# Kernel optimization log

Hardware: AMD Instinct MI355X
Metric: run time of the kernel (lower is better)

## Reference

```python
import jax, jax.numpy as jnp
import numpy as np

B, C, M, N = 8, 64, 256, 256
THRESHOLD = 0.8
EPS = 1e-5
PAD = 3  # kernel_size=7


def conv2d(x, w, b=None):
    # x: (B,Cin,H,W), w: (Cout,Cin,7,7), stride 1, 'same' padding 3
    y = jax.lax.conv_general_dilated(
        x, w, window_strides=(1, 1), padding=[(PAD, PAD), (PAD, PAD)],
        dimension_numbers=('NCHW', 'OIHW', 'NCHW'))
    if b is not None:
        y = y + b[None, :, None, None]
    return y


def region_norm(region, mask):
    # region: (B,C,M,N) zeroed outside region; mask: (B,C,M,N) binary
    s = jnp.sum(region, axis=(0, 2, 3))            # (C,)
    Sr = jnp.sum(mask, axis=(0, 2, 3))             # (C,)
    Sr = jnp.where(Sr == 0, 1.0, Sr)
    mu = (s / Sr)[None, :, None, None]
    t = region + (1.0 - mask) * mu                 # fill surroundings with region mean
    # BatchNorm2d(affine=False, track_running_stats=False): batch stats, biased var
    m = jnp.mean(t, axis=(0, 2, 3), keepdims=True)
    v = jnp.mean((t - m) ** 2, axis=(0, 2, 3), keepdims=True)
    bn = (t - m) * jax.lax.rsqrt(v + EPS)
    scale = jnp.sqrt(Sr / (region.shape[0] * region.shape[2] * region.shape[3]))
    return bn * scale[None, :, None, None]


def setup_inputs() -> dict:
    key = jax.random.key(0)
    k = jax.random.split(key, 6)
    x = jax.random.normal(k[0], (B, C, M, N), dtype=jnp.float32)
    # conv1: Conv2d(2,1,7,bias=False); gamma/beta: Conv2d(1,1,7) with bias
    w1 = jax.random.normal(k[1], (1, 2, 7, 7), dtype=jnp.float32) * 0.1
    wg = jax.random.normal(k[2], (1, 1, 7, 7), dtype=jnp.float32) * 0.1
    bg = jax.random.normal(k[3], (1,), dtype=jnp.float32) * 0.1
    wb = jax.random.normal(k[4], (1, 1, 7, 7), dtype=jnp.float32) * 0.1
    bb = jax.random.normal(k[5], (1,), dtype=jnp.float32) * 0.1
    return {"x": x, "w1": w1, "wg": wg, "bg": bg, "wb": wb, "bb": bb}


def reference(x, w1, wg, bg, wb, bb):
    # SelfAware_Affine
    avg_out = jnp.mean(x, axis=1, keepdims=True)       # (B,1,M,N)
    max_out = jnp.max(x, axis=1, keepdims=True)        # (B,1,M,N)
    sa_in = jnp.concatenate([avg_out, max_out], axis=1)
    sa_map = jax.nn.sigmoid(conv2d(sa_in, w1))         # (B,1,M,N)
    gamma = conv2d(sa_map, wg, bg)                     # (B,1,M,N)
    beta = conv2d(sa_map, wb, bb)                      # (B,1,M,N)
    # binary mask from detached importance map, expanded over channels
    mask = (jax.lax.stop_gradient(sa_map) >= THRESHOLD).astype(x.dtype)
    mask = jnp.broadcast_to(mask, x.shape)             # (B,C,M,N)
    rn_x = region_norm(x * mask, mask) + region_norm(x * (1.0 - mask), 1.0 - mask)
    return rn_x * (1.0 + gamma) + beta
```

## Files before the change

### kernel.cpp

```cpp
#include <hip/hip_runtime.h>
#include <cmath>

#define B_ 8
#define C_ 64
#define M_ 256
#define N_ 256
#define PLANE_ (M_*N_)
#define PIX_ (B_*PLANE_)
#define THRESH_ 0.8f
#define EPS_ 1e-5f

typedef float vfloat4 __attribute__((ext_vector_type(4)));

__global__ void k_avgmax(const float* __restrict__ x,
                         float* __restrict__ avgp, float* __restrict__ maxp) {
    int idx4 = (blockIdx.x * blockDim.x + threadIdx.x) * 4;
    int b = idx4 >> 16;
    int p = idx4 & (PLANE_ - 1);
    const float* xb = x + (size_t)b * C_ * PLANE_ + p;
    float4 s = make_float4(0.f, 0.f, 0.f, 0.f);
    float4 mx = make_float4(-INFINITY, -INFINITY, -INFINITY, -INFINITY);
    #pragma unroll 16
    for (int c = 0; c < C_; ++c) {
        float4 v = *(const float4*)(xb + (size_t)c * PLANE_);
        s.x += v.x; s.y += v.y; s.z += v.z; s.w += v.w;
        mx.x = fmaxf(mx.x, v.x); mx.y = fmaxf(mx.y, v.y);
        mx.z = fmaxf(mx.z, v.z); mx.w = fmaxf(mx.w, v.w);
    }
    const float r = 1.f / C_;
    s.x *= r; s.y *= r; s.z *= r; s.w *= r;
    *(float4*)(avgp + idx4) = s;
    *(float4*)(maxp + idx4) = mx;
}

__global__ void k_saconv(const float* __restrict__ avgp, const float* __restrict__ maxp,
                         const float* __restrict__ w1, float* __restrict__ samap,
                         unsigned char* __restrict__ maskp, int* __restrict__ cntp) {
    __shared__ float w[98];
    if (threadIdx.x < 98) w[threadIdx.x] = w1[threadIdx.x];
    __syncthreads();
    int idx = blockIdx.x * blockDim.x + threadIdx.x;
    int b = idx >> 16;
    int r = idx & (PLANE_ - 1);
    int i = r >> 8;
    int j = r & (N_ - 1);
    const float* a = avgp + (size_t)b * PLANE_;
    const float* m = maxp + (size_t)b * PLANE_;
    float acc = 0.f;
    #pragma unroll
    for (int dh = 0; dh < 7; ++dh) {
        int ii = i + dh - 3;
        if ((unsigned)ii >= (unsigned)M_) continue;
        #pragma unroll
        for (int dw = 0; dw < 7; ++dw) {
            int jj = j + dw - 3;
            if ((unsigned)jj >= (unsigned)N_) continue;
            int o = ii * N_ + jj;
            acc += a[o] * w[dh * 7 + dw] + m[o] * w[49 + dh * 7 + dw];
        }
    }
    float sa = 1.f / (1.f + expf(-acc));
    samap[idx] = sa;
    int mk = (sa >= THRESH_) ? 1 : 0;
    maskp[idx] = (unsigned char)mk;
    unsigned long long bal = __ballot(mk);
    __shared__ int wcnt[4];
    int wave = threadIdx.x >> 6, lane = threadIdx.x & 63;
    if (lane == 0) wcnt[wave] = __popcll(bal);
    __syncthreads();
    if (threadIdx.x == 0) atomicAdd(cntp, wcnt[0] + wcnt[1] + wcnt[2] + wcnt[3]);
}

__global__ void k_gammabeta(const float* __restrict__ samap,
                            const float* __restrict__ wg, const float* __restrict__ bgp,
                            const float* __restrict__ wb, const float* __restrict__ bbp,
                            float* __restrict__ gammap, float* __restrict__ betap) {
    __shared__ float w[98];
    if (threadIdx.x < 49) w[threadIdx.x] = wg[threadIdx.x];
    else if (threadIdx.x < 98) w[threadIdx.x] = wb[threadIdx.x - 49];
    __syncthreads();
    int idx = blockIdx.x * blockDim.x + threadIdx.x;
    int b = idx >> 16;
    int r = idx & (PLANE_ - 1);
    int i = r >> 8;
    int j = r & (N_ - 1);
    const float* s = samap + (size_t)b * PLANE_;
    float g = 0.f, be = 0.f;
    #pragma unroll
    for (int dh = 0; dh < 7; ++dh) {
        int ii = i + dh - 3;
        if ((unsigned)ii >= (unsigned)M_) continue;
        #pragma unroll
        for (int dw = 0; dw < 7; ++dw) {
            int jj = j + dw - 3;
            if ((unsigned)jj >= (unsigned)N_) continue;
            float v = s[ii * N_ + jj];
            g  += v * w[dh * 7 + dw];
            be += v * w[49 + dh * 7 + dw];
        }
    }
    gammap[idx] = g + bgp[0];
    betap[idx]  = be + bbp[0];
}

__global__ void k_sums(const float* __restrict__ x, const unsigned char* __restrict__ maskp,
                       float* __restrict__ S, float* __restrict__ Q,
                       float* __restrict__ S1, float* __restrict__ Q1) {
    int c = blockIdx.x;
    int chunk = blockIdx.y;
    int b = blockIdx.z;
    const float* xp = x + ((size_t)(b * C_ + c)) * PLANE_ + chunk * 8192;
    const unsigned char* mp = maskp + (size_t)b * PLANE_ + chunk * 8192;
    float s = 0.f, q = 0.f, s1 = 0.f, q1 = 0.f;
    #pragma unroll
    for (int k = 0; k < 8; ++k) {
        int t = (k * 256 + threadIdx.x) * 4;
        float4 v = *(const float4*)(xp + t);
        uchar4 mm = *(const uchar4*)(mp + t);
        float m0 = (float)mm.x, m1 = (float)mm.y, m2 = (float)mm.z, m3 = (float)mm.w;
        s  += v.x + v.y + v.z + v.w;
        q  += v.x * v.x + v.y * v.y + v.z * v.z + v.w * v.w;
        s1 += v.x * m0 + v.y * m1 + v.z * m2 + v.w * m3;
        q1 += v.x * v.x * m0 + v.y * v.y * m1 + v.z * v.z * m2 + v.w * v.w * m3;
    }
    for (int off = 32; off > 0; off >>= 1) {
        s  += __shfl_down(s, off, 64);
        q  += __shfl_down(q, off, 64);
        s1 += __shfl_down(s1, off, 64);
        q1 += __shfl_down(q1, off, 64);
    }
    __shared__ float ls[4][4];
    int wave = threadIdx.x >> 6, lane = threadIdx.x & 63;
    if (lane == 0) { ls[wave][0] = s; ls[wave][1] = q; ls[wave][2] = s1; ls[wave][3] = q1; }
    __syncthreads();
    if (threadIdx.x == 0) {
        float ts = 0.f, tq = 0.f, ts1 = 0.f, tq1 = 0.f;
        #pragma unroll
        for (int wv = 0; wv < 4; ++wv) { ts += ls[wv][0]; tq += ls[wv][1]; ts1 += ls[wv][2]; tq1 += ls[wv][3]; }
        atomicAdd(&S[c], ts); atomicAdd(&Q[c], tq);
        atomicAdd(&S1[c], ts1); atomicAdd(&Q1[c], tq1);
    }
}

__global__ void k_final(const float* __restrict__ x, const unsigned char* __restrict__ maskp,
                        const float* __restrict__ gammap, const float* __restrict__ betap,
                        const float* __restrict__ S, const float* __restrict__ Q,
                        const float* __restrict__ S1, const float* __restrict__ Q1,
                        const int* __restrict__ cntp,
                        float* __restrict__ out) {
    int c = blockIdx.x;
    int b = blockIdx.z;
    int p0 = blockIdx.y * 1024 + threadIdx.x * 4;

    const float P = (float)PIX_;
    int cnt1 = *cntp;
    float fc1 = (float)cnt1;
    float fc0 = P - fc1;
    float Sr1 = (cnt1 == 0) ? 1.f : fc1;
    float Sr0 = (cnt1 == PIX_) ? 1.f : fc0;
    float Sv = S[c], Qv = Q[c], S1v = S1[c], Q1v = Q1[c];
    float S0v = Sv - S1v, Q0v = Qv - Q1v;
    float mu1 = S1v / Sr1;
    float mu0 = S0v / Sr0;
    float m1 = (S1v + fc0 * mu1) / P;
    float v1 = fmaxf((Q1v + fc0 * mu1 * mu1) / P - m1 * m1, 0.f);
    float m0 = (S0v + fc1 * mu0) / P;
    float v0 = fmaxf((Q0v + fc1 * mu0 * mu0) / P - m0 * m0, 0.f);
    float A1 = rsqrtf(v1 + EPS_) * sqrtf(Sr1 / P);
    float A0 = rsqrtf(v0 + EPS_) * sqrtf(Sr0 / P);
    float B1 = (mu1 - m1) * A1;
    float B0 = (mu0 - m0) * A0;
    float ma = A1, mb = -m1 * A1 + B0;
    float ua = A0, ub = -m0 * A0 + B1;

    size_t base = ((size_t)(b * C_ + c)) * PLANE_ + p0;
    int pp = b * PLANE_ + p0;
    float4 xv = *(const float4*)(x + base);
    float4 gv = *(const float4*)(gammap + pp);
    float4 bv = *(const float4*)(betap + pp);
    uchar4 mv = *(const uchar4*)(maskp + pp);
    vfloat4 o;
    o.x = (mv.x ? xv.x * ma + mb : xv.x * ua + ub) * (1.f + gv.x) + bv.x;
    o.y = (mv.y ? xv.y * ma + mb : xv.y * ua + ub) * (1.f + gv.y) + bv.y;
    o.z = (mv.z ? xv.z * ma + mb : xv.z * ua + ub) * (1.f + gv.z) + bv.z;
    o.w = (mv.w ? xv.w * ma + mb : xv.w * ua + ub) * (1.f + gv.w) + bv.w;
    __builtin_nontemporal_store(o, (vfloat4*)(out + base));
}

extern "C" void kernel_launch(void* const* d_in, const int* in_sizes, int n_in,
                              void* d_out, int out_size, void* d_ws, size_t ws_size,
                              hipStream_t stream) {
    const float* x  = (const float*)d_in[0];
    const float* w1 = (const float*)d_in[1];
    const float* wg = (const float*)d_in[2];
    const float* bg = (const float*)d_in[3];
    const float* wb = (const float*)d_in[4];
    const float* bb = (const float*)d_in[5];
    float* out = (float*)d_out;

    float* ws = (float*)d_ws;
    float* avgp   = ws;
    float* maxp   = avgp + PIX_;
    float* samap  = maxp + PIX_;
    float* gammap = samap + PIX_;
    float* betap  = gammap + PIX_;
    float* S   = betap + PIX_;
    float* Q   = S + C_;
    float* S1  = Q + C_;
    float* Q1  = S1 + C_;
    int*   cnt = (int*)(Q1 + C_);
    unsigned char* maskp = (unsigned char*)(cnt + 1);

    (void)hipMemsetAsync(S, 0, (4 * C_ + 1) * sizeof(float), stream);

    k_avgmax<<<PIX_ / (256 * 4), 256, 0, stream>>>(x, avgp, maxp);
    k_saconv<<<PIX_ / 256, 256, 0, stream>>>(avgp, maxp, w1, samap, maskp, cnt);
    k_gammabeta<<<PIX_ / 256, 256, 0, stream>>>(samap, wg, bg, wb, bb, gammap, betap);
    dim3 g3(C_, 8, B_);
    k_sums<<<g3, 256, 0, stream>>>(x, maskp, S, Q, S1, Q1);
    dim3 g5(C_, PLANE_ / 1024, B_);
    k_final<<<g5, 256, 0, stream>>>(x, maskp, gammap, betap, S, Q, S1, Q1, cnt, out);
}
```

Measured before the change: 350.7 us.

## Fuse all stages into one cooperative persistent kernel with grid syncs

Replaces the five separate launches and the memset with a single cooperative kernel of 512 blocks that runs avg/max, SA conv, gamma/beta conv, channel sums and the final affine, separated by grid.sync barriers. The mask count now comes from the sums pass instead of a ballot plus atomic in the SA conv, and the accumulators are zeroed inside the kernel. The aim is to remove launch gaps and the memset. In exchange, each phase runs on a fixed grid that may leave bandwidth unused, and grid barriers have their own cost. The original multi-kernel path is kept as a fallback if the cooperative launch fails.

```diff
diff --git a/kernel.cpp b/kernel.cpp
--- a/kernel.cpp
+++ b/kernel.cpp
@@ -1,16 +1,211 @@
 #include <hip/hip_runtime.h>
+#include <hip/hip_cooperative_groups.h>
 #include <cmath>
+
+namespace cg = cooperative_groups;
 
 #define B_ 8
 #define C_ 64
 #define M_ 256
 #define N_ 256
-#define PLANE_ (M_*N_)
-#define PIX_ (B_*PLANE_)
+#define PLANE_ 65536
+#define PIX_ 524288
 #define THRESH_ 0.8f
 #define EPS_ 1e-5f
+#define NBLK_ 512
+#define NTHR_ 256
+#define NTID_ (NBLK_*NTHR_)
 
 typedef float vfloat4 __attribute__((ext_vector_type(4)));
+
+__global__ void __launch_bounds__(NTHR_, 2)
+k_mega(const float* __restrict__ x,
+       const float* __restrict__ w1, const float* __restrict__ wg,
+       const float* __restrict__ bgp, const float* __restrict__ wb,
+       const float* __restrict__ bbp,
+       float* __restrict__ avgp, float* __restrict__ maxp,
+       float* __restrict__ samap, float* __restrict__ gammap,
+       float* __restrict__ betap,
+       float* __restrict__ acc,
+       unsigned char* __restrict__ maskp,
+       float* __restrict__ out)
+{
+    cg::grid_group grid = cg::this_grid();
+    const int tid = blockIdx.x * NTHR_ + threadIdx.x;
+
+    __shared__ float w[196];
+    if (threadIdx.x < 98) w[threadIdx.x] = w1[threadIdx.x];
+    else if (threadIdx.x < 147) w[threadIdx.x] = wg[threadIdx.x - 98];
+    else if (threadIdx.x < 196) w[threadIdx.x] = wb[threadIdx.x - 147];
+
+    if (blockIdx.x == 0 && threadIdx.x < 257) acc[threadIdx.x] = 0.f;
+
+    {
+        int idx4 = tid * 4;
+        int b = idx4 >> 16;
+        int p = idx4 & (PLANE_ - 1);
+        const float* xb = x + (size_t)b * C_ * PLANE_ + p;
+        float4 s = make_float4(0.f, 0.f, 0.f, 0.f);
+        float4 mx = make_float4(-INFINITY, -INFINITY, -INFINITY, -INFINITY);
+        #pragma unroll 8
+        for (int c = 0; c < C_; ++c) {
+            float4 v = *(const float4*)(xb + (size_t)c * PLANE_);
+            s.x += v.x; s.y += v.y; s.z += v.z; s.w += v.w;
+            mx.x = fmaxf(mx.x, v.x); mx.y = fmaxf(mx.y, v.y);
+            mx.z = fmaxf(mx.z, v.z); mx.w = fmaxf(mx.w, v.w);
+        }
+        const float r = 1.f / C_;
+        s.x *= r; s.y *= r; s.z *= r; s.w *= r;
+        *(float4*)(avgp + idx4) = s;
+        *(float4*)(maxp + idx4) = mx;
+    }
+    grid.sync();
+
+    for (int px = tid; px < PIX_; px += NTID_) {
+        int b = px >> 16;
+        int r = px & (PLANE_ - 1);
+        int i = r >> 8;
+        int j = r & (N_ - 1);
+        const float* a = avgp + (size_t)b * PLANE_;
+        const float* m = maxp + (size_t)b * PLANE_;
+        float acc_ = 0.f;
+        #pragma unroll
+        for (int dh = 0; dh < 7; ++dh) {
+            int ii = i + dh - 3;
+            if ((unsigned)ii >= (unsigned)M_) continue;
+            #pragma unroll
+            for (int dw = 0; dw < 7; ++dw) {
+                int jj = j + dw - 3;
+                if ((unsigned)jj >= (unsigned)N_) continue;
+                int o = ii * N_ + jj;
+                acc_ += a[o] * w[dh * 7 + dw] + m[o] * w[49 + dh * 7 + dw];
+            }
+        }
+        float sa = 1.f / (1.f + expf(-acc_));
+        samap[px] = sa;
+        maskp[px] = (unsigned char)(sa >= THRESH_ ? 1 : 0);
+    }
+    grid.sync();
+
+    {
+        float bgv = bgp[0], bbv = bbp[0];
+        for (int px = tid; px < PIX_; px += NTID_) {
+            int b = px >> 16;
+            int r = px & (PLANE_ - 1);
+            int i = r >> 8;
+            int j = r & (N_ - 1);
+            const float* s = samap + (size_t)b * PLANE_;
+            float g = 0.f, be = 0.f;
+            #pragma unroll
+            for (int dh = 0; dh < 7; ++dh) {
+                int ii = i + dh - 3;
+                if ((unsigned)ii >= (unsigned)M_) continue;
+                #pragma unroll
+                for (int dw = 0; dw < 7; ++dw) {
+                    int jj = j + dw - 3;
+                    if ((unsigned)jj >= (unsigned)N_) continue;
+                    float v = s[ii * N_ + jj];
+                    g  += v * w[98 + dh * 7 + dw];
+                    be += v * w[147 + dh * 7 + dw];
+                }
+            }
+            gammap[px] = g + bgv;
+            betap[px]  = be + bbv;
+        }
+    }
+
+    {
+        __shared__ float ls[4][5];
+        for (int t = blockIdx.x; t < B_ * C_ * 8; t += NBLK_) {
+            int c = t & 63, chunk = (t >> 6) & 7, b = t >> 9;
+            const float* xp = x + ((size_t)(b * C_ + c)) * PLANE_ + chunk * 8192;
+            const unsigned char* mp = maskp + (size_t)b * PLANE_ + chunk * 8192;
+            float s = 0.f, q = 0.f, s1 = 0.f, q1 = 0.f, cn = 0.f;
+            #pragma unroll
+            for (int k = 0; k < 8; ++k) {
+                int o = (k * 256 + threadIdx.x) * 4;
+                float4 v = *(const float4*)(xp + o);
+                uchar4 mm = *(const uchar4*)(mp + o);
+                float m0 = (float)mm.x, m1 = (float)mm.y, m2 = (float)mm.z, m3 = (float)mm.w;
+                s  += v.x + v.y + v.z + v.w;
+                q  += v.x * v.x + v.y * v.y + v.z * v.z + v.w * v.w;
+                s1 += v.x * m0 + v.y * m1 + v.z * m2 + v.w * m3;
+                q1 += v.x * v.x * m0 + v.y * v.y * m1 + v.z * v.z * m2 + v.w * v.w * m3;
+                cn += m0 + m1 + m2 + m3;
+            }
+            for (int off = 32; off > 0; off >>= 1) {
+                s  += __shfl_down(s, off, 64);
+                q  += __shfl_down(q, off, 64);
+                s1 += __shfl_down(s1, off, 64);
+                q1 += __shfl_down(q1, off, 64);
+                cn += __shfl_down(cn, off, 64);
+            }
+            int wave = threadIdx.x >> 6, lane = threadIdx.x & 63;
+            if (lane == 0) {
+                ls[wave][0] = s; ls[wave][1] = q; ls[wave][2] = s1;
+                ls[wave][3] = q1; ls[wave][4] = cn;
+            }
+            __syncthreads();
+            if (threadIdx.x == 0) {
+                float ts = 0.f, tq = 0.f, ts1 = 0.f, tq1 = 0.f, tc = 0.f;
+                #pragma unroll
+                for (int wv = 0; wv < 4; ++wv) {
+                    ts += ls[wv][0]; tq += ls[wv][1]; ts1 += ls[wv][2];
+                    tq1 += ls[wv][3]; tc += ls[wv][4];
+                }
+                atomicAdd(&acc[c], ts); atomicAdd(&acc[64 + c], tq);
+                atomicAdd(&acc[128 + c], ts1); atomicAdd(&acc[192 + c], tq1);
+                if (c == 0) atomicAdd(&acc[256], tc);
+            }
+            __syncthreads();
+        }
+    }
+    __threadfence();
+    grid.sync();
+
+    {
+        int c = blockIdx.x & 63;
+        const float P = (float)PIX_;
+        float cntf = acc[256];
+        int cnt1 = (int)cntf;
+        float fc1 = cntf;
+        float fc0 = P - fc1;
+        float Sr1 = (cnt1 == 0) ? 1.f : fc1;
+        float Sr0 = (cnt1 == PIX_) ? 1.f : fc0;
+        float Sv = acc[c], Qv = acc[64 + c], S1v = acc[128 + c], Q1v = acc[192 + c];
+        float S0v = Sv - S1v, Q0v = Qv - Q1v;
+        float mu1 = S1v / Sr1;
+        float mu0 = S0v / Sr0;
+        float m1 = (S1v + fc0 * mu1) / P;
+        float v1 = fmaxf((Q1v + fc0 * mu1 * mu1) / P - m1 * m1, 0.f);
+        float m0 = (S0v + fc1 * mu0) / P;
+        float v0 = fmaxf((Q0v + fc1 * mu0 * mu0) / P - m0 * m0, 0.f);
+        float A1 = rsqrtf(v1 + EPS_) * sqrtf(Sr1 / P);
+        float A0 = rsqrtf(v0 + EPS_) * sqrtf(Sr0 / P);
+        float B1c = (mu1 - m1) * A1;
+        float B0c = (mu0 - m0) * A0;
+        float ma = A1, mb = -m1 * A1 + B0c;
+        float ua = A0, ub = -m0 * A0 + B1c;
+
+        for (int t = blockIdx.x; t < B_ * C_ * 64; t += NBLK_) {
+            int chunk = (t >> 6) & 63;
+            int b = t >> 12;
+            int p0 = chunk * 1024 + threadIdx.x * 4;
+            size_t base = ((size_t)(b * C_ + c)) * PLANE_ + p0;
+            int pp = b * PLANE_ + p0;
+            float4 xv = *(const float4*)(x + base);
+            float4 gv = *(const float4*)(gammap + pp);
+            float4 bv = *(const float4*)(betap + pp);
+            uchar4 mv = *(const uchar4*)(maskp + pp);
+            vfloat4 o;
+            o.x = (mv.x ? xv.x * ma + mb : xv.x * ua + ub) * (1.f + gv.x) + bv.x;
+            o.y = (mv.y ? xv.y * ma + mb : xv.y * ua + ub) * (1.f + gv.y) + bv.y;
+            o.z = (mv.z ? xv.z * ma + mb : xv.z * ua + ub) * (1.f + gv.z) + bv.z;
+            o.w = (mv.w ? xv.w * ma + mb : xv.w * ua + ub) * (1.f + gv.w) + bv.w;
+            __builtin_nontemporal_store(o, (vfloat4*)(out + base));
+        }
+    }
+}
 
 __global__ void k_avgmax(const float* __restrict__ x,
                          float* __restrict__ avgp, float* __restrict__ maxp) {
@@ -35,7 +230,7 @@
 
 __global__ void k_saconv(const float* __restrict__ avgp, const float* __restrict__ maxp,
                          const float* __restrict__ w1, float* __restrict__ samap,
-                         unsigned char* __restrict__ maskp, int* __restrict__ cntp) {
+                         unsigned char* __restrict__ maskp) {
     __shared__ float w[98];
     if (threadIdx.x < 98) w[threadIdx.x] = w1[threadIdx.x];
     __syncthreads();
@@ -61,14 +256,7 @@
     }
     float sa = 1.f / (1.f + expf(-acc));
     samap[idx] = sa;
-    int mk = (sa >= THRESH_) ? 1 : 0;
-    maskp[idx] = (unsigned char)mk;
-    unsigned long long bal = __ballot(mk);
-    __shared__ int wcnt[4];
-    int wave = threadIdx.x >> 6, lane = threadIdx.x & 63;
-    if (lane == 0) wcnt[wave] = __popcll(bal);
-    __syncthreads();
-    if (threadIdx.x == 0) atomicAdd(cntp, wcnt[0] + wcnt[1] + wcnt[2] + wcnt[3]);
+    maskp[idx] = (unsigned char)(sa >= THRESH_ ? 1 : 0);
 }
 
 __global__ void k_gammabeta(const float* __restrict__ samap,
@@ -104,14 +292,13 @@
 }
 
 __global__ void k_sums(const float* __restrict__ x, const unsigned char* __restrict__ maskp,
-                       float* __restrict__ S, float* __restrict__ Q,
-                       float* __restrict__ S1, float* __restrict__ Q1) {
+                       float* __restrict__ acc) {
     int c = blockIdx.x;
     int chunk = blockIdx.y;
     int b = blockIdx.z;
     const float* xp = x + ((size_t)(b * C_ + c)) * PLANE_ + chunk * 8192;
     const unsigned char* mp = maskp + (size_t)b * PLANE_ + chunk * 8192;
-    float s = 0.f, q = 0.f, s1 = 0.f, q1 = 0.f;
+    float s = 0.f, q = 0.f, s1 = 0.f, q1 = 0.f, cn = 0.f;
     #pragma unroll
     for (int k = 0; k < 8; ++k) {
         int t = (k * 256 + threadIdx.x) * 4;
@@ -122,43 +309,46 @@
         q  += v.x * v.x + v.y * v.y + v.z * v.z + v.w * v.w;
         s1 += v.x * m0 + v.y * m1 + v.z * m2 + v.w * m3;
         q1 += v.x * v.x * m0 + v.y * v.y * m1 + v.z * v.z * m2 + v.w * v.w * m3;
+        cn += m0 + m1 + m2 + m3;
     }
     for (int off = 32; off > 0; off >>= 1) {
         s  += __shfl_down(s, off, 64);
         q  += __shfl_down(q, off, 64);
         s1 += __shfl_down(s1, off, 64);
         q1 += __shfl_down(q1, off, 64);
-    }
-    __shared__ float ls[4][4];
+        cn += __shfl_down(cn, off, 64);
+    }
+    __shared__ float ls[4][5];
     int wave = threadIdx.x >> 6, lane = threadIdx.x & 63;
-    if (lane == 0) { ls[wave][0] = s; ls[wave][1] = q; ls[wave][2] = s1; ls[wave][3] = q1; }
+    if (lane == 0) { ls[wave][0] = s; ls[wave][1] = q; ls[wave][2] = s1; ls[wave][3] = q1; ls[wave][4] = cn; }
     __syncthreads();
     if (threadIdx.x == 0) {
-        float ts = 0.f, tq = 0.f, ts1 = 0.f, tq1 = 0.f;
+        float ts = 0.f, tq = 0.f, ts1 = 0.f, tq1 = 0.f, tc = 0.f;
         #pragma unroll
-        for (int wv = 0; wv < 4; ++wv) { ts += ls[wv][0]; tq += ls[wv][1]; ts1 += ls[wv][2]; tq1 += ls[wv][3]; }
-        atomicAdd(&S[c], ts); atomicAdd(&Q[c], tq);
-        atomicAdd(&S1[c], ts1); atomicAdd(&Q1[c], tq1);
+        for (int wv = 0; wv < 4; ++wv) {
+            ts += ls[wv][0]; tq += ls[wv][1]; ts1 += ls[wv][2]; tq1 += ls[wv][3]; tc += ls[wv][4];
+        }
+        atomicAdd(&acc[c], ts); atomicAdd(&acc[64 + c], tq);
+        atomicAdd(&acc[128 + c], ts1); atomicAdd(&acc[192 + c], tq1);
+        if (c == 0) atomicAdd(&acc[256], tc);
     }
 }
 
 __global__ void k_final(const float* __restrict__ x, const unsigned char* __restrict__ maskp,
                         const float* __restrict__ gammap, const float* __restrict__ betap,
-                        const float* __restrict__ S, const float* __restrict__ Q,
-                        const float* __restrict__ S1, const float* __restrict__ Q1,
-                        const int* __restrict__ cntp,
-                        float* __restrict__ out) {
+                        const float* __restrict__ acc, float* __restrict__ out) {
     int c = blockIdx.x;
     int b = blockIdx.z;
     int p0 = blockIdx.y * 1024 + threadIdx.x * 4;
 
     const float P = (float)PIX_;
-    int cnt1 = *cntp;
-    float fc1 = (float)cnt1;
+    float cntf = acc[256];
+    int cnt1 = (int)cntf;
+    float fc1 = cntf;
     float fc0 = P - fc1;
     float Sr1 = (cnt1 == 0) ? 1.f : fc1;
     float Sr0 = (cnt1 == PIX_) ? 1.f : fc0;
-    float Sv = S[c], Qv = Q[c], S1v = S1[c], Q1v = Q1[c];
+    float Sv = acc[c], Qv = acc[64 + c], S1v = acc[128 + c], Q1v = acc[192 + c];
     float S0v = Sv - S1v, Q0v = Qv - Q1v;
     float mu1 = S1v / Sr1;
     float mu0 = S0v / Sr0;
@@ -168,10 +358,10 @@
     float v0 = fmaxf((Q0v + fc1 * mu0 * mu0) / P - m0 * m0, 0.f);
     float A1 = rsqrtf(v1 + EPS_) * sqrtf(Sr1 / P);
     float A0 = rsqrtf(v0 + EPS_) * sqrtf(Sr0 / P);
-    float B1 = (mu1 - m1) * A1;
-    float B0 = (mu0 - m0) * A0;
-    float ma = A1, mb = -m1 * A1 + B0;
-    float ua = A0, ub = -m0 * A0 + B1;
+    float B1c = (mu1 - m1) * A1;
+    float B0c = (mu0 - m0) * A0;
+    float ma = A1, mb = -m1 * A1 + B0c;
+    float ua = A0, ub = -m0 * A0 + B1c;
 
     size_t base = ((size_t)(b * C_ + c)) * PLANE_ + p0;
     int pp = b * PLANE_ + p0;
@@ -204,20 +394,22 @@
     float* samap  = maxp + PIX_;
     float* gammap = samap + PIX_;
     float* betap  = gammap + PIX_;
-    float* S   = betap + PIX_;
-    float* Q   = S + C_;
-    float* S1  = Q + C_;
-    float* Q1  = S1 + C_;
-    int*   cnt = (int*)(Q1 + C_);
-    unsigned char* maskp = (unsigned char*)(cnt + 1);
-
-    (void)hipMemsetAsync(S, 0, (4 * C_ + 1) * sizeof(float), stream);
-
-    k_avgmax<<<PIX_ / (256 * 4), 256, 0, stream>>>(x, avgp, maxp);
-    k_saconv<<<PIX_ / 256, 256, 0, stream>>>(avgp, maxp, w1, samap, maskp, cnt);
-    k_gammabeta<<<PIX_ / 256, 256, 0, stream>>>(samap, wg, bg, wb, bb, gammap, betap);
-    dim3 g3(C_, 8, B_);
-    k_sums<<<g3, 256, 0, stream>>>(x, maskp, S, Q, S1, Q1);
-    dim3 g5(C_, PLANE_ / 1024, B_);
-    k_final<<<g5, 256, 0, stream>>>(x, maskp, gammap, betap, S, Q, S1, Q1, cnt, out);
-}
+    float* acc    = betap + PIX_;
+    unsigned char* maskp = (unsigned char*)(acc + 260);
+
+    void* args[] = { (void*)&x, (void*)&w1, (void*)&wg, (void*)&bg, (void*)&wb, (void*)&bb,
+                     (void*)&avgp, (void*)&maxp, (void*)&samap, (void*)&gammap, (void*)&betap,
+                     (void*)&acc, (void*)&maskp, (void*)&out };
+    hipError_t e = hipLaunchCooperativeKernel((const void*)k_mega, dim3(NBLK_), dim3(NTHR_),
+                                              args, 0, stream);
+    if (e != hipSuccess) {
+        (void)hipMemsetAsync(acc, 0, 257 * sizeof(float), stream);
+        k_avgmax<<<PIX_ / (256 * 4), 256, 0, stream>>>(x, avgp, maxp);
+        k_saconv<<<PIX_ / 256, 256, 0, stream>>>(avgp, maxp, w1, samap, maskp);
+        k_gammabeta<<<PIX_ / 256, 256, 0, stream>>>(samap, wg, bg, wb, bb, gammap, betap);
+        dim3 g3(C_, 8, B_);
+        k_sums<<<g3, 256, 0, stream>>>(x, maskp, acc);
+        dim3 g5(C_, PLANE_ / 1024, B_);
+        k_final<<<g5, 256, 0, stream>>>(x, maskp, gammap, betap, acc, out);
+    }
+}
```

New measurement: 604.2 us. +72.3%, slower.
